# Kernel optimization log

Hardware: AMD Instinct MI355X
Metric: run time of the kernel (lower is better)

The kernel has to match this reference:

```python
import jax, jax.numpy as jnp
import numpy as np

HS = WS = 1024      # downsampled mask dims (8192 / scale_factor 8)
K = 24              # kernel_num
KD = 35             # kernel_dim1 == kernel_dim2
OFF = HS // 2 - KD // 2  # offset_s = 495
MASK_STEEP = 4.0
MASK_SHIFT = 0.5
RESIST_STEEP = 50.0
RESIST_TH = 0.225
MAX_DOSE = 1.02
MIN_DOSE = 0.98
POOL = 3            # avepool_kernel


def setup_inputs() -> dict:
    key = jax.random.key(0)
    ks = jax.random.split(key, 7)
    return {
        "mask_s": jax.random.uniform(ks[0], (1, 1, HS, WS), dtype=jnp.float32),
        "kf_re": jax.random.normal(ks[1], (K, KD, KD), dtype=jnp.float32),
        "kf_im": jax.random.normal(ks[2], (K, KD, KD), dtype=jnp.float32),
        "kd_re": jax.random.normal(ks[3], (K, KD, KD), dtype=jnp.float32),
        "kd_im": jax.random.normal(ks[4], (K, KD, KD), dtype=jnp.float32),
        "kf_scale": jax.random.uniform(ks[5], (K, 1, 1), dtype=jnp.float32),
        "kd_scale": jax.random.uniform(ks[6], (K, 1, 1), dtype=jnp.float32),
    }


def _avgpool3(x):
    # AvgPool2d(kernel=3, stride=1, pad=1), count_include_pad=True -> always /9
    s = jax.lax.reduce_window(x, 0.0, jax.lax.add, (1, 1, POOL, POOL),
                              (1, 1, 1, 1),
                              [(0, 0), (0, 0), (POOL // 2, POOL // 2), (POOL // 2, POOL // 2)])
    return s / float(POOL * POOL)


def _dose_branch(crop, kernel, scale, dose):
    # crop: [1,1,KD,KD] complex ; kernel: [K,KD,KD] complex ; scale: [K,1,1]
    buf = jnp.zeros((1, K, HS, WS), dtype=jnp.complex64)
    buf = buf.at[:, :, OFF:OFF + KD, OFF:OFF + KD].set(crop * dose * kernel)
    img = jnp.fft.ifft2(buf)                      # [1,K,HS,WS] complex
    inten = (img.real * img.real + img.imag * img.imag) * scale
    inten = jnp.sum(inten, axis=1, keepdims=True)  # [1,1,HS,WS]
    return jax.nn.sigmoid(RESIST_STEEP * (inten - RESIST_TH))


def reference(mask_s, kf_re, kf_im, kd_re, kd_im, kf_scale, kd_scale):
    kf = jax.lax.complex(kf_re, kf_im)
    kd = jax.lax.complex(kd_re, kd_im)
    mask = jax.nn.sigmoid(MASK_STEEP * (_avgpool3(mask_s) - MASK_SHIFT))
    mf = jnp.fft.fftshift(jnp.fft.fft2(mask), axes=(-2, -1))  # [1,1,HS,WS]
    crop = mf[:, :, OFF:OFF + KD, OFF:OFF + KD]               # [1,1,KD,KD]
    x_nom = _dose_branch(crop, kf, kf_scale, 1.0)
    x_max = _dose_branch(crop, kf, kf_scale, MAX_DOSE)
    x_min = _dose_branch(crop, kd, kd_scale, MIN_DOSE)
    return x_nom, x_max, x_min
```

## Files before the change

kernel.cpp:

```cpp
#include <hip/hip_runtime.h>
#include <math.h>

#define HS 1024
#define WS 1024
#define KK 24
#define KD 35
#define NF 35
#define NDP 69
#define NGRP 16
#define CROW 42
#define PROW 37

#define G_OFF    0u
#define CROP_OFF 286720u
#define D_OFF    296520u
#define ZERO_QWORDS 6055

__global__ __launch_bounds__(256) void k_maskG(const float* __restrict__ ms,
                                               float2* __restrict__ G,
                                               unsigned long long* __restrict__ zq) {
    __shared__ float cs[WS + 8];
    __shared__ float m[WS];
    __shared__ float2 part[252];
    const int x = blockIdx.x;
    const int t = threadIdx.x;

    if (x < 24) {
        int i = x * 256 + t;
        if (i < ZERO_QWORDS) zq[i] = 0ull;
    }
    {
        const int j = 4 * t;
        float4 b = *(const float4*)&ms[x * WS + j];
        float4 a = make_float4(0.f, 0.f, 0.f, 0.f);
        float4 d = make_float4(0.f, 0.f, 0.f, 0.f);
        if (x > 0)      a = *(const float4*)&ms[(x - 1) * WS + j];
        if (x < HS - 1) d = *(const float4*)&ms[(x + 1) * WS + j];
        float4 s;
        s.x = a.x + b.x + d.x;
        s.y = a.y + b.y + d.y;
        s.z = a.z + b.z + d.z;
        s.w = a.w + b.w + d.w;
        *(float4*)&cs[4 + j] = s;
        if (t == 0) { cs[3] = 0.0f; cs[4 + WS] = 0.0f; }
    }
    __syncthreads();
    {
        const int j = 4 * t;
        float4 c = *(const float4*)&cs[4 + j];
        float l = cs[3 + j];
        float r = cs[8 + j];
        float p0 = (l   + c.x + c.y) * (1.0f / 9.0f);
        float p1 = (c.x + c.y + c.z) * (1.0f / 9.0f);
        float p2 = (c.y + c.z + c.w) * (1.0f / 9.0f);
        float p3 = (c.z + c.w + r  ) * (1.0f / 9.0f);
        float4 mv;
        mv.x = 1.0f / (1.0f + expf(-4.0f * (p0 - 0.5f)));
        mv.y = 1.0f / (1.0f + expf(-4.0f * (p1 - 0.5f)));
        mv.z = 1.0f / (1.0f + expf(-4.0f * (p2 - 0.5f)));
        mv.w = 1.0f / (1.0f + expf(-4.0f * (p3 - 0.5f)));
        *(float4*)&m[j] = mv;
    }
    __syncthreads();
    if (t < 252) {
        const int qi = t / 14, seg = t % 14;
        float si, ci, ss, cc;
        sincospif(-(float)(qi * seg) * (1.0f / 512.0f), &si, &ci);
        sincospif(-(float)(qi * 14)  * (1.0f / 512.0f), &ss, &cc);
        float wr = ci, wi = si;
        float re = 0.0f, im = 0.0f;
        for (int y = seg; y < WS; y += 14) {
            float mv = m[y];
            re += mv * wr;
            im += mv * wi;
            float nr = wr * cc - wi * ss;
            wi = wr * ss + wi * cc;
            wr = nr;
        }
        part[t] = make_float2(re, im);
    }
    __syncthreads();
    if (t < 18) {
        float re = 0.0f, im = 0.0f;
        for (int s = 0; s < 14; ++s) { float2 p = part[t * 14 + s]; re += p.x; im += p.y; }
        G[(17 + t) * HS + x] = make_float2(re, im);
        if (t > 0) G[(17 - t) * HS + x] = make_float2(re, -im);
    }
}

__global__ __launch_bounds__(256) void k_crop(const float2* __restrict__ G,
                                              float2* __restrict__ crop) {
    __shared__ float2 g2[128];
    __shared__ float2 part[245];
    const int q  = blockIdx.x >> 3;
    const int xs = (blockIdx.x & 7) * 128;
    const int t  = threadIdx.x;
    if (t < 128) g2[t] = G[q * HS + xs + t];
    __syncthreads();
    if (t < 245) {
        const int p = t / 7, seg = t % 7;
        const int v = p - 17;
        float si, ci, ss, cc;
        sincospif((float)(v * (xs + seg)) * (1.0f / 512.0f), &si, &ci);
        sincospif((float)(v * 7)          * (1.0f / 512.0f), &ss, &cc);
        float wr = ci, wi = si;
        float re = 0.0f, im = 0.0f;
        for (int r = seg; r < 128; r += 7) {
            float2 gv = g2[r];
            re += gv.x * wr + gv.y * wi;
            im += gv.y * wr - gv.x * wi;
            float nr = wr * cc - wi * ss;
            wi = wr * ss + wi * cc;
            wr = nr;
        }
        part[t] = make_float2(re, im);
    }
    __syncthreads();
    if (t < NF) {
        float re = 0.0f, im = 0.0f;
        for (int s = 0; s < 7; ++s) { float2 p2 = part[t * 7 + s]; re += p2.x; im += p2.y; }
        float* dst = (float*)&crop[t * NF + q];
        atomicAdd(dst,     re);
        atomicAdd(dst + 1, im);
    }
}

__global__ __launch_bounds__(256) void k_D(
    const float2* __restrict__ crop,
    const float* __restrict__ kre0, const float* __restrict__ kim0,
    const float* __restrict__ kre1, const float* __restrict__ kim1,
    const float* __restrict__ sc0,  const float* __restrict__ sc1,
    float2* __restrict__ D)
{
    __shared__ float2 C[KD * CROW];
    __shared__ float2 partR[28 * PROW];
    const int tup = blockIdx.x;
    const int t   = threadIdx.x;

    const int b   = tup / (KK * NGRP);
    const int rem = tup % (KK * NGRP);
    const int k   = rem / NGRP;
    const int g   = rem % NGRP;
    const float* kre = b ? kre1 : kre0;
    const float* kim = b ? kim1 : kim0;
    const float dosefac = (b ? 0.98f : 1.0f) * (1.0f / 1048576.0f);
    const float sk2 = ((b ? sc1 : sc0)[k]) * dosefac * dosefac;

    if (t < 245) C[(t / 7) * CROW + 35 + (t % 7)] = make_float2(0.0f, 0.0f);
    #pragma unroll
    for (int j = 0; j < 5; ++j) {
        int i = t + j * 256;
        if (i < KD * KD) {
            float2 c = crop[i];
            int row = i / 35, col = i % 35;
            float kr = kre[k * KD * KD + i], ki = kim[k * KD * KD + i];
            C[row * CROW + col] = make_float2(c.x * kr - c.y * ki,
                                              c.x * ki + c.y * kr);
        }
    }
    __syncthreads();

    const int tile = t / 28;
    const int r    = t % 28;
    const int pgrp = r / 7;
    const int useg = r % 7;
    const int d0   = tile * 4;
    const int u0   = useg * 5;

    for (int idp = g; idp < NDP; idp += NGRP) {
        const int dp = idp - 34;
        if (t < 252) {
            const int plo = max(0, dp), phi = min(34, 34 + dp);
            float2 ac0 = {0,0}, ac1 = {0,0}, ac2 = {0,0}, ac3 = {0,0};
            if (u0 <= 34 - d0) {
                for (int p = plo + pgrp; p <= phi; p += 4) {
                    const float2* rowa = &C[p * CROW + d0 + u0];
                    const float2* rowb = &C[(p - dp) * CROW + u0];
                    float2 a0 = rowa[0], a1 = rowa[1], a2 = rowa[2];
                    #pragma unroll
                    for (int s = 0; s < 5; ++s) {
                        float2 a3 = rowa[s + 3];
                        float2 bb = rowb[s];
                        ac0.x += a0.x * bb.x + a0.y * bb.y;  ac0.y += a0.y * bb.x - a0.x * bb.y;
                        ac1.x += a1.x * bb.x + a1.y * bb.y;  ac1.y += a1.y * bb.x - a1.x * bb.y;
                        ac2.x += a2.x * bb.x + a2.y * bb.y;  ac2.y += a2.y * bb.x - a2.x * bb.y;
                        ac3.x += a3.x * bb.x + a3.y * bb.y;  ac3.y += a3.y * bb.x - a3.x * bb.y;
                        a0 = a1; a1 = a2; a2 = a3;
                    }
                }
            }
            const int base = r * PROW + d0;
            partR[base]     = ac0;
            partR[base + 1] = ac1;
            partR[base + 2] = ac2;
            partR[base + 3] = ac3;
        }
        __syncthreads();
        if (t < NF) {
            float re = 0.0f, im = 0.0f;
            for (int rr = 0; rr < 28; ++rr) {
                float2 v = partR[rr * PROW + t];
                re += v.x; im += v.y;
            }
            float* dst = (float*)&D[(b * NDP + idp) * NF + t];
            atomicAdd(dst,     re * sk2);
            atomicAdd(dst + 1, im * sk2);
        }
        __syncthreads();
    }
}

__global__ __launch_bounds__(256) void k_final(const float2* __restrict__ D,
                                               float* __restrict__ out) {
    __shared__ float2 partB[210];
    __shared__ float2 B[2][NF];
    const int x = blockIdx.x;
    const int t = threadIdx.x;
    if (t < 210) {
        const int s = t / 70, r = t % 70, b = r / 35, dq = r % 35;
        float si, ci, ss, cc;
        sincospif((float)((23 * s - 34) * x) * (1.0f / 512.0f), &si, &ci);
        sincospif((float)x                   * (1.0f / 512.0f), &ss, &cc);
        float wr = ci, wi = si;
        float re = 0.0f, im = 0.0f;
        const int i0 = 23 * s;
        for (int idp = i0; idp < i0 + 23; ++idp) {
            float2 d = D[(b * NDP + idp) * NF + dq];
            re += d.x * wr - d.y * wi;
            im += d.x * wi + d.y * wr;
            float nr = wr * cc - wi * ss;
            wi = wr * ss + wi * cc;
            wr = nr;
        }
        partB[t] = make_float2(re, im);
    }
    __syncthreads();
    if (t < 70) {
        float2 a = partB[t], b2 = partB[t + 70], c = partB[t + 140];
        B[t / 35][t % 35] = make_float2(a.x + b2.x + c.x, a.y + b2.y + c.y);
    }
    __syncthreads();
    const float bf0 = B[0][0].x;
    const float bd0 = B[1][0].x;
    float s1, c1;
    sincospif((float)t * (1.0f / 512.0f), &s1, &c1);
    float cx = c1, cy = s1;
    float sf[4] = {0.f, 0.f, 0.f, 0.f};
    float sd[4] = {0.f, 0.f, 0.f, 0.f};
    #pragma unroll
    for (int dq = 1; dq < NF; ++dq) {
        const float2 bf = B[0][dq];
        const float2 bd = B[1][dq];
        const float Pfx = bf.x * cx - bf.y * cy;
        const float Pfy = bf.x * cy + bf.y * cx;
        const float Pdx = bd.x * cx - bd.y * cy;
        const float Pdy = bd.x * cy + bd.y * cx;
        #pragma unroll
        for (int j = 0; j < 4; ++j) {
            const int s = (dq * j) & 3;
            sf[j] += (s == 0) ? Pfx : (s == 1) ? -Pfy : (s == 2) ? -Pfx : Pfy;
            sd[j] += (s == 0) ? Pdx : (s == 1) ? -Pdy : (s == 2) ? -Pdx : Pdy;
        }
        const float nx = cx * c1 - cy * s1;
        cy = cx * s1 + cy * c1;
        cx = nx;
    }
    #pragma unroll
    for (int j = 0; j < 4; ++j) {
        const float If = bf0 + 2.0f * sf[j];
        const float Id = bd0 + 2.0f * sd[j];
        const int o = x * WS + t + 256 * j;
        out[o]               = 1.0f / (1.0f + expf(-50.0f * (If - 0.225f)));
        out[o + HS * WS]     = 1.0f / (1.0f + expf(-50.0f * (1.0404f * If - 0.225f)));
        out[o + 2 * HS * WS] = 1.0f / (1.0f + expf(-50.0f * (Id - 0.225f)));
    }
}

extern "C" void kernel_launch(void* const* d_in, const int* in_sizes, int n_in,
                              void* d_out, int out_size, void* d_ws, size_t ws_size,
                              hipStream_t stream) {
    (void)in_sizes; (void)n_in; (void)out_size; (void)ws_size;
    const float* ms    = (const float*)d_in[0];
    const float* kf_re = (const float*)d_in[1];
    const float* kf_im = (const float*)d_in[2];
    const float* kd_re = (const float*)d_in[3];
    const float* kd_im = (const float*)d_in[4];
    const float* kf_sc = (const float*)d_in[5];
    const float* kd_sc = (const float*)d_in[6];

    char* ws = (char*)d_ws;
    float2* G      = (float2*)(ws + G_OFF);
    float2* crop   = (float2*)(ws + CROP_OFF);
    float2* D      = (float2*)(ws + D_OFF);
    unsigned long long* zq = (unsigned long long*)(ws + CROP_OFF);
    float* out     = (float*)d_out;

    k_maskG<<<HS, 256, 0, stream>>>(ms, G, zq);
    k_crop<<<NF * 8, 256, 0, stream>>>(G, crop);
    k_D<<<2 * KK * NGRP, 256, 0, stream>>>(crop, kf_re, kf_im, kd_re, kd_im, kf_sc, kd_sc, D);
    k_final<<<HS, 256, 0, stream>>>(D, out);
}
```

Before: 52.65 us.

## Fold DFT symmetries in maskG/final, split crop finer, double-buffer k_D partials

k_maskG folds the 1024-point partial DFT into 256 iterations by combining the four quarter-period samples with ±1/±i twiddles. k_final accumulates the four output phases by dq mod 4 and recombines them at the end, replacing per-j select chains. k_crop splits each row into 16 chunks of 64 instead of 8 of 128, and k_D double-buffers the partial buffer to drop one barrier per iteration. Together these cut arithmetic and sync work, at the cost of more atomics in k_crop and some extra rounding from reassociation.

```diff
diff --git a/kernel.cpp b/kernel.cpp
--- a/kernel.cpp
+++ b/kernel.cpp
@@ -67,12 +67,20 @@
         float si, ci, ss, cc;
         sincospif(-(float)(qi * seg) * (1.0f / 512.0f), &si, &ci);
         sincospif(-(float)(qi * 14)  * (1.0f / 512.0f), &ss, &cc);
+        const float s2 = (qi & 1) ? -1.0f : 1.0f;
+        const int qm = qi & 3;
+        const float er = (qm == 0) ? 1.0f : (qm == 2) ? -1.0f : 0.0f;
+        const float ei = (qm == 1) ? -1.0f : (qm == 3) ? 1.0f : 0.0f;
         float wr = ci, wi = si;
         float re = 0.0f, im = 0.0f;
-        for (int y = seg; y < WS; y += 14) {
-            float mv = m[y];
-            re += mv * wr;
-            im += mv * wi;
+        for (int y = seg; y < 256; y += 14) {
+            float m0 = m[y], m1 = m[y + 256], m2 = m[y + 512], m3 = m[y + 768];
+            float A  = fmaf(s2, m2, m0);
+            float Bv = fmaf(s2, m3, m1);
+            float tre = fmaf(er, Bv, A);
+            float tim = ei * Bv;
+            re += tre * wr - tim * wi;
+            im += tre * wi + tim * wr;
             float nr = wr * cc - wi * ss;
             wi = wr * ss + wi * cc;
             wr = nr;
@@ -90,12 +98,12 @@
 
 __global__ __launch_bounds__(256) void k_crop(const float2* __restrict__ G,
                                               float2* __restrict__ crop) {
-    __shared__ float2 g2[128];
+    __shared__ float2 g2[64];
     __shared__ float2 part[245];
-    const int q  = blockIdx.x >> 3;
-    const int xs = (blockIdx.x & 7) * 128;
+    const int q  = blockIdx.x >> 4;
+    const int xs = (blockIdx.x & 15) * 64;
     const int t  = threadIdx.x;
-    if (t < 128) g2[t] = G[q * HS + xs + t];
+    if (t < 64) g2[t] = G[q * HS + xs + t];
     __syncthreads();
     if (t < 245) {
         const int p = t / 7, seg = t % 7;
@@ -105,7 +113,7 @@
         sincospif((float)(v * 7)          * (1.0f / 512.0f), &ss, &cc);
         float wr = ci, wi = si;
         float re = 0.0f, im = 0.0f;
-        for (int r = seg; r < 128; r += 7) {
+        for (int r = seg; r < 64; r += 7) {
             float2 gv = g2[r];
             re += gv.x * wr + gv.y * wi;
             im += gv.y * wr - gv.x * wi;
@@ -133,7 +141,7 @@
     float2* __restrict__ D)
 {
     __shared__ float2 C[KD * CROW];
-    __shared__ float2 partR[28 * PROW];
+    __shared__ float2 partR[2][28 * PROW];
     const int tup = blockIdx.x;
     const int t   = threadIdx.x;
 
@@ -167,6 +175,7 @@
     const int d0   = tile * 4;
     const int u0   = useg * 5;
 
+    int pb = 0;
     for (int idp = g; idp < NDP; idp += NGRP) {
         const int dp = idp - 34;
         if (t < 252) {
@@ -190,30 +199,30 @@
                 }
             }
             const int base = r * PROW + d0;
-            partR[base]     = ac0;
-            partR[base + 1] = ac1;
-            partR[base + 2] = ac2;
-            partR[base + 3] = ac3;
+            partR[pb][base]     = ac0;
+            partR[pb][base + 1] = ac1;
+            partR[pb][base + 2] = ac2;
+            partR[pb][base + 3] = ac3;
         }
         __syncthreads();
         if (t < NF) {
             float re = 0.0f, im = 0.0f;
             for (int rr = 0; rr < 28; ++rr) {
-                float2 v = partR[rr * PROW + t];
+                float2 v = partR[pb][rr * PROW + t];
                 re += v.x; im += v.y;
             }
             float* dst = (float*)&D[(b * NDP + idp) * NF + t];
             atomicAdd(dst,     re * sk2);
             atomicAdd(dst + 1, im * sk2);
         }
-        __syncthreads();
+        pb ^= 1;
     }
 }
 
 __global__ __launch_bounds__(256) void k_final(const float2* __restrict__ D,
                                                float* __restrict__ out) {
     __shared__ float2 partB[210];
-    __shared__ float2 B[2][NF];
+    __shared__ float2 B[NF][2];
     const int x = blockIdx.x;
     const int t = threadIdx.x;
     if (t < 210) {
@@ -237,34 +246,38 @@
     __syncthreads();
     if (t < 70) {
         float2 a = partB[t], b2 = partB[t + 70], c = partB[t + 140];
-        B[t / 35][t % 35] = make_float2(a.x + b2.x + c.x, a.y + b2.y + c.y);
+        B[t % 35][t / 35] = make_float2(a.x + b2.x + c.x, a.y + b2.y + c.y);
     }
     __syncthreads();
     const float bf0 = B[0][0].x;
-    const float bd0 = B[1][0].x;
+    const float bd0 = B[0][1].x;
     float s1, c1;
     sincospif((float)t * (1.0f / 512.0f), &s1, &c1);
     float cx = c1, cy = s1;
-    float sf[4] = {0.f, 0.f, 0.f, 0.f};
-    float sd[4] = {0.f, 0.f, 0.f, 0.f};
+    float2 Sf[4] = {{0,0},{0,0},{0,0},{0,0}};
+    float2 Sd[4] = {{0,0},{0,0},{0,0},{0,0}};
     #pragma unroll
     for (int dq = 1; dq < NF; ++dq) {
-        const float2 bf = B[0][dq];
-        const float2 bd = B[1][dq];
-        const float Pfx = bf.x * cx - bf.y * cy;
-        const float Pfy = bf.x * cy + bf.y * cx;
-        const float Pdx = bd.x * cx - bd.y * cy;
-        const float Pdy = bd.x * cy + bd.y * cx;
-        #pragma unroll
-        for (int j = 0; j < 4; ++j) {
-            const int s = (dq * j) & 3;
-            sf[j] += (s == 0) ? Pfx : (s == 1) ? -Pfy : (s == 2) ? -Pfx : Pfy;
-            sd[j] += (s == 0) ? Pdx : (s == 1) ? -Pdy : (s == 2) ? -Pdx : Pdy;
-        }
+        const float2 bf = B[dq][0];
+        const float2 bd = B[dq][1];
+        const int mm = dq & 3;
+        Sf[mm].x += bf.x * cx - bf.y * cy;
+        Sf[mm].y += bf.x * cy + bf.y * cx;
+        Sd[mm].x += bd.x * cx - bd.y * cy;
+        Sd[mm].y += bd.x * cy + bd.y * cx;
         const float nx = cx * c1 - cy * s1;
         cy = cx * s1 + cy * c1;
         cx = nx;
     }
+    float sf[4], sd[4];
+    sf[0] = Sf[0].x + Sf[1].x + Sf[2].x + Sf[3].x;
+    sf[1] = Sf[0].x - Sf[1].y - Sf[2].x + Sf[3].y;
+    sf[2] = Sf[0].x - Sf[1].x + Sf[2].x - Sf[3].x;
+    sf[3] = Sf[0].x + Sf[1].y - Sf[2].x - Sf[3].y;
+    sd[0] = Sd[0].x + Sd[1].x + Sd[2].x + Sd[3].x;
+    sd[1] = Sd[0].x - Sd[1].y - Sd[2].x + Sd[3].y;
+    sd[2] = Sd[0].x - Sd[1].x + Sd[2].x - Sd[3].x;
+    sd[3] = Sd[0].x + Sd[1].y - Sd[2].x - Sd[3].y;
     #pragma unroll
     for (int j = 0; j < 4; ++j) {
         const float If = bf0 + 2.0f * sf[j];
@@ -296,7 +309,7 @@
     float* out     = (float*)d_out;
 
     k_maskG<<<HS, 256, 0, stream>>>(ms, G, zq);
-    k_crop<<<NF * 8, 256, 0, stream>>>(G, crop);
+    k_crop<<<NF * 16, 256, 0, stream>>>(G, crop);
     k_D<<<2 * KK * NGRP, 256, 0, stream>>>(crop, kf_re, kf_im, kd_re, kd_im, kf_sc, kd_sc, D);
     k_final<<<HS, 256, 0, stream>>>(D, out);
 }
```

After: 51.65 us. About the same (-1.9%).
